# Kernel tuning notes

Measured on AMD Instinct MI355X. Metric: run time of the kernel, lower is better.

## Reference

```python
import jax, jax.numpy as jnp
import numpy as np

SEQ = 4096
D_EMB = 2048
D_HEAD = 128
SCALE = 0.02


def setup_inputs() -> dict:
    key = jax.random.key(0)
    kx, kq, kk, kv, ko = jax.random.split(key, 5)
    x = jax.random.normal(kx, (SEQ, D_EMB), dtype=jnp.float32)
    W_Q = jax.random.normal(kq, (D_EMB, D_EMB), dtype=jnp.float32) * SCALE
    W_K = jax.random.normal(kk, (D_EMB, D_EMB), dtype=jnp.float32) * SCALE
    W_V = jax.random.normal(kv, (D_EMB, D_EMB), dtype=jnp.float32) * SCALE
    W_O = jax.random.normal(ko, (D_EMB, D_EMB), dtype=jnp.float32) * SCALE
    b_Q = jnp.zeros((D_EMB,), dtype=jnp.float32)
    b_K = jnp.zeros((D_EMB,), dtype=jnp.float32)
    b_V = jnp.zeros((D_EMB,), dtype=jnp.float32)
    b_O = jnp.zeros((D_EMB,), dtype=jnp.float32)
    return {"x": x, "W_Q": W_Q, "W_K": W_K, "W_V": W_V, "W_O": W_O,
            "b_Q": b_Q, "b_K": b_K, "b_V": b_V, "b_O": b_O, "d_head": D_HEAD}


def reference(x, W_Q, W_K, W_V, W_O, b_Q, b_K, b_V, b_O, d_head):
    # x: [S, D]
    q = x @ W_Q + b_Q  # [S, D]
    k = x @ W_K + b_K
    v = x @ W_V + b_V
    scores = (q @ k.T) / jnp.sqrt(jnp.float32(d_head))  # [S, S]
    seq = scores.shape[0]
    causal = jnp.tril(jnp.ones((seq, seq), dtype=bool))
    scores = jnp.where(causal, scores, -jnp.inf)
    weights = jax.nn.softmax(scores, axis=-1)  # [S, S]
    attn_out = weights @ v  # [S, D]
    return attn_out @ W_O + b_O
```

## Files before the change

### kernel.cpp

```cpp
#include <hip/hip_runtime.h>
#include <hip/hip_fp16.h>

typedef _Float16 f16;
typedef _Float16 f16x8 __attribute__((ext_vector_type(8)));
typedef _Float16 f16x4 __attribute__((ext_vector_type(4)));
typedef float    f32x4 __attribute__((ext_vector_type(4)));

#define SEQ      4096
#define DEMB     2048
#define SCALE_QK 0.08838834764831845f

#define GAS __attribute__((address_space(1)))
#define LAS __attribute__((address_space(3)))

__device__ __forceinline__ void load_lds16(const f16* g, f16* l) {
    __builtin_amdgcn_global_load_lds((const GAS void*)g, (LAS void*)l, 16, 0, 0);
}

__device__ __forceinline__ f16x8 ldsr(const f16* base, int byteoff) {
    byteoff ^= (byteoff >> 3) & 0x70;
    return *(const f16x8*)((const char*)base + byteoff);
}

__device__ __forceinline__ void stage_half(const f16* __restrict__ src, int ldk,
                                           f16* ldsdst, int tid) {
#pragma unroll
    for (int s = 0; s < 2; ++s) {
        const int o   = s * 8192 + tid * 16;
        const int osw = o ^ ((o >> 3) & 0x70);
        load_lds16(src + (size_t)(osw >> 7) * ldk + ((osw & 127) >> 1),
                   ldsdst + (s * 8192 + (tid >> 6) * 1024) / 2);
    }
}

template <int MODE>
__device__ __forceinline__ void gemm_core(
        const f16* __restrict__ A, int lda, const f16* __restrict__ BT, int ldb,
        void* __restrict__ outp, int ldo, const float* __restrict__ bias,
        int bm, int bn, int NTc, int kt0, float scale, f16* lds) {
    const int m0 = bm * 256, n0 = bn * 256;
    const int NI = NTc >> 1;

    const int tid  = threadIdx.x;
    const int lane = tid & 63;
    const int wr   = (tid >> 6) >> 2;
    const int wc   = (tid >> 6) & 3;
    const int fr   = lane & 15;
    const int kb   = (lane >> 4) * 16;

    const f16* Abase = A + (size_t)m0 * lda + kt0 * 64;
    const f16* Bbase = BT + (size_t)n0 * ldb + kt0 * 64;

#define STG(buf, isB, half, t) \
    stage_half((isB) ? (Bbase + (size_t)((half) * 128) * ldb + (t) * 64) \
                     : (Abase + (size_t)((half) * 128) * lda + (t) * 64), \
               (isB) ? ldb : lda, \
               lds + (buf) * 32768 + (isB) * 16384 + (half) * 8192, tid)

    f32x4 acc[8][4] = {};
    f16x8 af[8], bf0[4], bf1[4];

#define READ_A(Mh, buf) { \
    const f16* bb = lds + (buf) * 32768; \
    _Pragma("unroll") for (int m = 0; m < 4; ++m) \
    _Pragma("unroll") for (int ks = 0; ks < 2; ++ks) \
        af[m * 2 + ks] = ldsr(bb, ((Mh) * 128 + wr * 64 + m * 16 + fr) * 128 + ks * 64 + kb); }

#define READ_B(Nh, buf, dst) { \
    const f16* bb = lds + (buf) * 32768 + 16384; \
    _Pragma("unroll") for (int n = 0; n < 2; ++n) \
    _Pragma("unroll") for (int ks = 0; ks < 2; ++ks) \
        dst[n * 2 + ks] = ldsr(bb, ((Nh) * 128 + wc * 32 + n * 16 + fr) * 128 + ks * 64 + kb); }

#define MFMA_PH(Mh, Nh, bfx) { \
    __builtin_amdgcn_s_setprio(1); \
    _Pragma("unroll") for (int m = 0; m < 4; ++m) \
    _Pragma("unroll") for (int n = 0; n < 2; ++n) \
    _Pragma("unroll") for (int ks = 0; ks < 2; ++ks) \
        acc[(Mh) * 4 + m][(Nh) * 2 + n] = __builtin_amdgcn_mfma_f32_16x16x32_f16( \
            af[m * 2 + ks], bfx[n * 2 + ks], acc[(Mh) * 4 + m][(Nh) * 2 + n], 0, 0, 0); \
    __builtin_amdgcn_s_setprio(0); }

#define BAR   asm volatile("s_barrier" ::: "memory")
#define VM6   asm volatile("s_waitcnt vmcnt(6)" ::: "memory")
#define VM0   asm volatile("s_waitcnt vmcnt(0)" ::: "memory")

    STG(0, 0, 0, 0); STG(0, 1, 0, 0); STG(0, 1, 1, 0); STG(0, 0, 1, 0);
    STG(1, 0, 0, 1); STG(1, 1, 0, 1); STG(1, 1, 1, 1);
    VM6; BAR;

    for (int i = 0; i < NI; ++i) {
        const int t0 = 2 * i;
        const bool more = (i + 1 < NI);
        READ_A(0, 0); READ_B(0, 0, bf0);
        STG(1, 0, 1, t0 + 1);
        BAR; MFMA_PH(0, 0, bf0); BAR;
        READ_B(1, 0, bf1);
        if (more) STG(0, 0, 0, t0 + 2);
        BAR; MFMA_PH(0, 1, bf1); BAR;
        READ_A(1, 0);
        if (more) STG(0, 1, 0, t0 + 2);
        BAR; MFMA_PH(1, 0, bf0); BAR;
        if (more) { STG(0, 1, 1, t0 + 2); VM6; } else { VM0; }
        BAR; MFMA_PH(1, 1, bf1); BAR;
        READ_A(0, 1); READ_B(0, 1, bf0);
        if (more) STG(0, 0, 1, t0 + 2);
        BAR; MFMA_PH(0, 0, bf0); BAR;
        READ_B(1, 1, bf1);
        if (more) STG(1, 0, 0, t0 + 3);
        BAR; MFMA_PH(0, 1, bf1); BAR;
        READ_A(1, 1);
        if (more) STG(1, 1, 0, t0 + 3);
        BAR; MFMA_PH(1, 0, bf0); BAR;
        if (more) STG(1, 1, 1, t0 + 3);
        VM6;
        BAR; MFMA_PH(1, 1, bf1); BAR;
    }

    const int rq = (lane >> 4) * 4;
#pragma unroll
    for (int mi = 0; mi < 8; ++mi) {
        const int row = m0 + (mi >> 2) * 128 + wr * 64 + (mi & 3) * 16 + rq;
#pragma unroll
        for (int ni = 0; ni < 4; ++ni) {
            const int col = n0 + (ni >> 1) * 128 + wc * 32 + (ni & 1) * 16 + fr;
            if (MODE == 0) {
                f16* o = (f16*)outp;
                const float bv = bias[col];
#pragma unroll
                for (int r = 0; r < 4; ++r)
                    o[(size_t)(row + r) * ldo + col] = (f16)(acc[mi][ni][r] + bv);
            } else if (MODE == 1) {
                f16* o = (f16*)outp;
                f16x4 v;
#pragma unroll
                for (int r = 0; r < 4; ++r) v[r] = (f16)acc[mi][ni][r];
                *(f16x4*)&o[(size_t)col * ldo + row] = v;
            } else if (MODE == 2) {
                float* o = (float*)outp;
                const float bv = bias ? bias[col] : 0.f;
#pragma unroll
                for (int r = 0; r < 4; ++r)
                    atomicAdd(&o[(size_t)(row + r) * ldo + col], acc[mi][ni][r] + bv);
            } else {
                f16* o = (f16*)outp;
#pragma unroll
                for (int r = 0; r < 4; ++r)
                    o[(size_t)(row + r) * ldo + col] = (f16)(acc[mi][ni][r] * scale);
            }
        }
    }
#undef STG
#undef READ_A
#undef READ_B
#undef MFMA_PH
#undef BAR
#undef VM6
#undef VM0
}

__global__ __launch_bounds__(256) void cvt_f16(const float* __restrict__ in,
                                               f16* __restrict__ out, int n) {
    int i = (blockIdx.x * 256 + threadIdx.x) * 4;
    if (i >= n) return;
    float4 v = *(const float4*)&in[i];
    f16x4 o; o[0] = (f16)v.x; o[1] = (f16)v.y; o[2] = (f16)v.z; o[3] = (f16)v.w;
    *(f16x4*)&out[i] = o;
}

__global__ __launch_bounds__(256) void transpose_cvt4(
        const float* __restrict__ WQ, const float* __restrict__ WK,
        const float* __restrict__ WV, const float* __restrict__ WO,
        f16* __restrict__ wqkvt, f16* __restrict__ wot) {
    __shared__ f16 tile[64][72];
    const int z = blockIdx.z;
    const float* in = z == 0 ? WQ : z == 1 ? WK : z == 2 ? WV : WO;
    f16* out = z < 3 ? wqkvt + (size_t)z * DEMB * DEMB : wot;
    const int c0 = blockIdx.x * 64, r0 = blockIdx.y * 64;
    const int tx = threadIdx.x & 63, ty = threadIdx.x >> 6;
    for (int rr = ty; rr < 64; rr += 4)
        tile[tx][rr] = (f16)in[(size_t)(r0 + rr) * DEMB + c0 + tx];
    __syncthreads();
    for (int cc = ty; cc < 64; cc += 4)
        out[(size_t)(c0 + cc) * DEMB + r0 + tx] = tile[cc][tx];
}

__global__ __launch_bounds__(512, 2)
void k_qkv(const f16* __restrict__ x16, const f16* __restrict__ wqkvt,
           f16* __restrict__ qkv16, const float* __restrict__ bqkv) {
    __shared__ f16 lds[65536];
    gemm_core<0>(x16, DEMB, wqkvt, DEMB, qkv16, 3 * DEMB, bqkv,
                 blockIdx.y, blockIdx.x, 32, 0, 1.f, lds);
}

__global__ __launch_bounds__(512, 2)
void k_scores(const f16* __restrict__ qkv16, f16* __restrict__ sb) {
    __shared__ f16 lds[65536];
    const int bid = blockIdx.x;
    int bm = (int)((sqrtf(8.f * bid + 1.f) - 1.f) * 0.5f);
    while ((bm + 1) * (bm + 2) / 2 <= bid) ++bm;
    while (bm * (bm + 1) / 2 > bid) --bm;
    const int bn = bid - bm * (bm + 1) / 2;
    gemm_core<3>(qkv16, 3 * DEMB, qkv16 + DEMB, 3 * DEMB, sb, SEQ, nullptr,
                 bm, bn, 32, 0, SCALE_QK, lds);
}

__global__ __launch_bounds__(512, 2)
void k_vw_softmax(const f16* __restrict__ qkv16, const f16* __restrict__ wot,
                  f16* __restrict__ vwT, f16* __restrict__ sb) {
    __shared__ f16 lds[65536];
    const int bid = blockIdx.x;
    if (bid < 128) {
        gemm_core<1>(qkv16 + 2 * DEMB, 3 * DEMB, wot, DEMB, vwT, SEQ, nullptr,
                     bid >> 3, bid & 7, 32, 0, 1.f, lds);
        return;
    }
    f16* srow = lds + (size_t)(threadIdx.x >> 8) * SEQ;
    float* red = (float*)(lds + 2 * SEQ);
    const int half = threadIdx.x >> 8;
    const int tt   = threadIdx.x & 255;
    const int i    = 2 * (bid - 128) + half;
    const int L    = i + 1;
    const int Lp   = ((i >> 8) + 1) << 8;
    f16* row = sb + (size_t)i * SEQ;

    float mx = -3.0e38f;
    for (int j0 = tt * 8; j0 < Lp; j0 += 2048) {
        f16x8 v = *(const f16x8*)&row[j0];
        *(f16x8*)&srow[j0] = v;
#pragma unroll
        for (int u = 0; u < 8; ++u)
            if (j0 + u < L) mx = fmaxf(mx, (float)v[u]);
    }
#pragma unroll
    for (int o = 32; o > 0; o >>= 1) mx = fmaxf(mx, __shfl_xor(mx, o));
    if ((tt & 63) == 0) red[half * 8 + (tt >> 6)] = mx;
    __syncthreads();
    mx = fmaxf(fmaxf(red[half * 8 + 0], red[half * 8 + 1]),
               fmaxf(red[half * 8 + 2], red[half * 8 + 3]));

    float sm = 0.f;
    for (int j0 = tt * 8; j0 < Lp; j0 += 2048) {
        f16x8 v = *(const f16x8*)&srow[j0];
#pragma unroll
        for (int u = 0; u < 8; ++u)
            if (j0 + u < L) sm += __expf((float)v[u] - mx);
    }
#pragma unroll
    for (int o = 32; o > 0; o >>= 1) sm += __shfl_xor(sm, o);
    if ((tt & 63) == 0) red[half * 8 + 4 + (tt >> 6)] = sm;
    __syncthreads();
    const float inv = 1.f / (red[half * 8 + 4] + red[half * 8 + 5] +
                             red[half * 8 + 6] + red[half * 8 + 7]);

    for (int j0 = tt * 8; j0 < Lp; j0 += 2048) {
        f16x8 v = *(const f16x8*)&srow[j0];
        f16x8 wv;
#pragma unroll
        for (int u = 0; u < 8; ++u)
            wv[u] = (j0 + u < L) ? (f16)(__expf((float)v[u] - mx) * inv) : (f16)0.f;
        *(f16x8*)&row[j0] = wv;
    }
}

__global__ __launch_bounds__(512, 2)
void k_pvw(const f16* __restrict__ sb, const f16* __restrict__ vwT,
           float* __restrict__ out, const float* __restrict__ bO) {
    __shared__ f16 lds[65536];
    const int bm = blockIdx.y, bn = blockIdx.x, z = blockIdx.z;
    const int NT = (bm + 1) * 4;
    const int half = NT >> 1;
    gemm_core<2>(sb, SEQ, vwT, SEQ, out, DEMB, z == 0 ? bO : nullptr,
                 bm, bn, half, z * half, 1.f, lds);
}

extern "C" void kernel_launch(void* const* d_in, const int* in_sizes, int n_in,
                              void* d_out, int out_size, void* d_ws, size_t ws_size,
                              hipStream_t stream) {
    const float* x  = (const float*)d_in[0];
    const float* WQ = (const float*)d_in[1];
    const float* WK = (const float*)d_in[2];
    const float* WV = (const float*)d_in[3];
    const float* WO = (const float*)d_in[4];
    const float* bQ = (const float*)d_in[5];
    const float* bK = (const float*)d_in[6];
    const float* bV = (const float*)d_in[7];
    const float* bO = (const float*)d_in[8];
    float* out = (float*)d_out;

    char* w = (char*)d_ws;
    f16* qkv16 = (f16*)w; w += (size_t)SEQ * 3 * DEMB * 2;
    f16* vwT   = (f16*)w; w += (size_t)DEMB * SEQ * 2;
    f16* wot   = (f16*)w; w += (size_t)DEMB * DEMB * 2;
    float* bqkv = (float*)w; w += 3 * DEMB * 4 + 8192;
    char* R = w;
    f16* x16   = (f16*)R;
    f16* wqkvt = (f16*)(R + (size_t)SEQ * DEMB * 2);
    f16* sb    = (f16*)R;

    cvt_f16<<<(SEQ * DEMB) / 1024, 256, 0, stream>>>(x, x16, SEQ * DEMB);
    transpose_cvt4<<<dim3(DEMB / 64, DEMB / 64, 4), 256, 0, stream>>>(
        WQ, WK, WV, WO, wqkvt, wot);
    hipMemcpyAsync(bqkv, bQ, DEMB * 4, hipMemcpyDeviceToDevice, stream);
    hipMemcpyAsync(bqkv + DEMB, bK, DEMB * 4, hipMemcpyDeviceToDevice, stream);
    hipMemcpyAsync(bqkv + 2 * DEMB, bV, DEMB * 4, hipMemcpyDeviceToDevice, stream);

    k_qkv<<<dim3(3 * DEMB / 256, SEQ / 256), 512, 0, stream>>>(
        x16, wqkvt, qkv16, bqkv);

    k_scores<<<136, 512, 0, stream>>>(qkv16, sb);

    k_vw_softmax<<<128 + SEQ / 2, 512, 0, stream>>>(qkv16, wot, vwT, sb);

    hipMemsetAsync(out, 0, (size_t)SEQ * DEMB * 4, stream);
    k_pvw<<<dim3(DEMB / 256, SEQ / 256, 2), 512, 0, stream>>>(sb, vwT, out, bO);
}
```

Measured before the change: 347.2 us.

## Fold W_V into W_O product and balance causal PV split across blocks

```diff
diff --git a/kernel.cpp b/kernel.cpp
--- a/kernel.cpp
+++ b/kernel.cpp
@@ -37,9 +37,8 @@
 __device__ __forceinline__ void gemm_core(
         const f16* __restrict__ A, int lda, const f16* __restrict__ BT, int ldb,
         void* __restrict__ outp, int ldo, const float* __restrict__ bias,
-        int bm, int bn, int NTc, int kt0, float scale, f16* lds) {
+        int bm, int bn, int NI, int kt0, float scale, f16* lds) {
     const int m0 = bm * 256, n0 = bn * 256;
-    const int NI = NTc >> 1;
 
     const int tid  = threadIdx.x;
     const int lane = tid & 63;
@@ -168,14 +167,14 @@
     *(f16x4*)&out[i] = o;
 }
 
-__global__ __launch_bounds__(256) void transpose_cvt4(
+__global__ __launch_bounds__(256) void transpose_cvt3(
         const float* __restrict__ WQ, const float* __restrict__ WK,
-        const float* __restrict__ WV, const float* __restrict__ WO,
-        f16* __restrict__ wqkvt, f16* __restrict__ wot) {
+        const float* __restrict__ WO,
+        f16* __restrict__ wqkt, f16* __restrict__ wot) {
     __shared__ f16 tile[64][72];
     const int z = blockIdx.z;
-    const float* in = z == 0 ? WQ : z == 1 ? WK : z == 2 ? WV : WO;
-    f16* out = z < 3 ? wqkvt + (size_t)z * DEMB * DEMB : wot;
+    const float* in = z == 0 ? WQ : z == 1 ? WK : WO;
+    f16* out = z == 0 ? wqkt : z == 1 ? wqkt + (size_t)DEMB * DEMB : wot;
     const int c0 = blockIdx.x * 64, r0 = blockIdx.y * 64;
     const int tx = threadIdx.x & 63, ty = threadIdx.x >> 6;
     for (int rr = ty; rr < 64; rr += 4)
@@ -186,33 +185,56 @@
 }
 
 __global__ __launch_bounds__(512, 2)
-void k_qkv(const f16* __restrict__ x16, const f16* __restrict__ wqkvt,
-           f16* __restrict__ qkv16, const float* __restrict__ bqkv) {
+void k_qk(const f16* __restrict__ x16, const f16* __restrict__ wqkt,
+          f16* __restrict__ qk16, const float* __restrict__ bqk) {
     __shared__ f16 lds[65536];
-    gemm_core<0>(x16, DEMB, wqkvt, DEMB, qkv16, 3 * DEMB, bqkv,
-                 blockIdx.y, blockIdx.x, 32, 0, 1.f, lds);
+    gemm_core<0>(x16, DEMB, wqkt, DEMB, qk16, 2 * DEMB, bqk,
+                 blockIdx.y, blockIdx.x, 16, 0, 1.f, lds);
 }
 
 __global__ __launch_bounds__(512, 2)
-void k_scores(const f16* __restrict__ qkv16, f16* __restrict__ sb) {
+void k_scores_wvo(const f16* __restrict__ qk16, f16* __restrict__ sb,
+                  const f16* __restrict__ wv16, const f16* __restrict__ wot,
+                  f16* __restrict__ wvoT) {
     __shared__ f16 lds[65536];
     const int bid = blockIdx.x;
-    int bm = (int)((sqrtf(8.f * bid + 1.f) - 1.f) * 0.5f);
-    while ((bm + 1) * (bm + 2) / 2 <= bid) ++bm;
-    while (bm * (bm + 1) / 2 > bid) --bm;
-    const int bn = bid - bm * (bm + 1) / 2;
-    gemm_core<3>(qkv16, 3 * DEMB, qkv16 + DEMB, 3 * DEMB, sb, SEQ, nullptr,
-                 bm, bn, 32, 0, SCALE_QK, lds);
+    if (bid < 136) {
+        int bm = (int)((sqrtf(8.f * bid + 1.f) - 1.f) * 0.5f);
+        while ((bm + 1) * (bm + 2) / 2 <= bid) ++bm;
+        while (bm * (bm + 1) / 2 > bid) --bm;
+        const int bn = bid - bm * (bm + 1) / 2;
+        gemm_core<3>(qk16, 2 * DEMB, qk16 + DEMB, 2 * DEMB, sb, SEQ, nullptr,
+                     bm, bn, 16, 0, SCALE_QK, lds);
+    } else {
+        const int w = bid - 136;
+        gemm_core<1>(wv16, DEMB, wot, DEMB, wvoT, DEMB, nullptr,
+                     w >> 3, w & 7, 16, 0, 1.f, lds);
+    }
 }
 
 __global__ __launch_bounds__(512, 2)
-void k_vw_softmax(const f16* __restrict__ qkv16, const f16* __restrict__ wot,
-                  f16* __restrict__ vwT, f16* __restrict__ sb) {
+void k_vw_sm_bias(const f16* __restrict__ x16, const f16* __restrict__ wvoT,
+                  f16* __restrict__ vwT, f16* __restrict__ sb,
+                  const float* __restrict__ WO, const float* __restrict__ bV,
+                  const float* __restrict__ bO, float* __restrict__ bc) {
     __shared__ f16 lds[65536];
     const int bid = blockIdx.x;
     if (bid < 128) {
-        gemm_core<1>(qkv16 + 2 * DEMB, 3 * DEMB, wot, DEMB, vwT, SEQ, nullptr,
-                     bid >> 3, bid & 7, 32, 0, 1.f, lds);
+        gemm_core<1>(x16, DEMB, wvoT, DEMB, vwT, SEQ, nullptr,
+                     bid >> 3, bid & 7, 16, 0, 1.f, lds);
+        return;
+    }
+    if (bid >= 2176) {
+        float* part = (float*)lds;
+        const int j0 = (bid - 2176) * 256;
+        const int jj = threadIdx.x & 255;
+        const int hf = threadIdx.x >> 8;
+        float acc = 0.f;
+        for (int i = hf * 1024; i < (hf + 1) * 1024; ++i)
+            acc += bV[i] * WO[(size_t)i * DEMB + j0 + jj];
+        part[hf * 256 + jj] = acc;
+        __syncthreads();
+        if (hf == 0) bc[j0 + jj] = part[jj] + part[256 + jj] + bO[j0 + jj];
         return;
     }
     f16* srow = lds + (size_t)(threadIdx.x >> 8) * SEQ;
@@ -265,13 +287,18 @@
 
 __global__ __launch_bounds__(512, 2)
 void k_pvw(const f16* __restrict__ sb, const f16* __restrict__ vwT,
-           float* __restrict__ out, const float* __restrict__ bO) {
+           float* __restrict__ out, const float* __restrict__ bc) {
     __shared__ f16 lds[65536];
-    const int bm = blockIdx.y, bn = blockIdx.x, z = blockIdx.z;
-    const int NT = (bm + 1) * 4;
-    const int half = NT >> 1;
-    gemm_core<2>(sb, SEQ, vwT, SEQ, out, DEMB, z == 0 ? bO : nullptr,
-                 bm, bn, half, z * half, 1.f, lds);
+    static const short BMt[30] = {0,1,2,3,4,5,6,6,7,7,8,8,9,9,10,10,11,11,
+                                  12,12,12,13,13,13,14,14,14,15,15,15};
+    static const short KT0t[30] = {0,0,0,0,0,0,0,14,0,16,0,18,0,20,0,22,0,24,
+                                   0,18,36,0,20,38,0,20,40,0,22,44};
+    static const short NIt[30] = {2,4,6,8,10,12,7,7,8,8,9,9,10,10,11,11,12,12,
+                                  9,9,8,10,9,9,10,10,10,11,11,10};
+    const int e = blockIdx.x, bn = blockIdx.y;
+    const int bm = BMt[e], kt0 = KT0t[e], ni = NIt[e];
+    gemm_core<2>(sb, SEQ, vwT, SEQ, out, DEMB, kt0 == 0 ? bc : nullptr,
+                 bm, bn, ni, kt0, 1.f, lds);
 }
 
 extern "C" void kernel_launch(void* const* d_in, const int* in_sizes, int n_in,
@@ -289,29 +316,31 @@
     float* out = (float*)d_out;
 
     char* w = (char*)d_ws;
-    f16* qkv16 = (f16*)w; w += (size_t)SEQ * 3 * DEMB * 2;
-    f16* vwT   = (f16*)w; w += (size_t)DEMB * SEQ * 2;
-    f16* wot   = (f16*)w; w += (size_t)DEMB * DEMB * 2;
-    float* bqkv = (float*)w; w += 3 * DEMB * 4 + 8192;
-    char* R = w;
-    f16* x16   = (f16*)R;
-    f16* wqkvt = (f16*)(R + (size_t)SEQ * DEMB * 2);
-    f16* sb    = (f16*)R;
+    f16* qk16 = (f16*)w; w += (size_t)SEQ * 2 * DEMB * 2;
+    f16* sb   = (f16*)w; w += (size_t)SEQ * SEQ * 2;
+    f16* x16  = (f16*)w; w += (size_t)SEQ * DEMB * 2;
+    f16* wqkt = (f16*)w; w += (size_t)2 * DEMB * DEMB * 2;
+    f16* wv16 = (f16*)w; w += (size_t)DEMB * DEMB * 2;
+    f16* wot  = (f16*)w; w += (size_t)DEMB * DEMB * 2;
+    f16* wvoT = (f16*)w; w += (size_t)DEMB * DEMB * 2;
+    float* bqk = (float*)w; w += 2 * DEMB * 4;
+    float* bc  = (float*)w; w += DEMB * 4 + 4096;
+    f16* vwT = wqkt;
 
     cvt_f16<<<(SEQ * DEMB) / 1024, 256, 0, stream>>>(x, x16, SEQ * DEMB);
-    transpose_cvt4<<<dim3(DEMB / 64, DEMB / 64, 4), 256, 0, stream>>>(
-        WQ, WK, WV, WO, wqkvt, wot);
-    hipMemcpyAsync(bqkv, bQ, DEMB * 4, hipMemcpyDeviceToDevice, stream);
-    hipMemcpyAsync(bqkv + DEMB, bK, DEMB * 4, hipMemcpyDeviceToDevice, stream);
-    hipMemcpyAsync(bqkv + 2 * DEMB, bV, DEMB * 4, hipMemcpyDeviceToDevice, stream);
-
-    k_qkv<<<dim3(3 * DEMB / 256, SEQ / 256), 512, 0, stream>>>(
-        x16, wqkvt, qkv16, bqkv);
-
-    k_scores<<<136, 512, 0, stream>>>(qkv16, sb);
-
-    k_vw_softmax<<<128 + SEQ / 2, 512, 0, stream>>>(qkv16, wot, vwT, sb);
+    cvt_f16<<<(DEMB * DEMB) / 1024, 256, 0, stream>>>(WV, wv16, DEMB * DEMB);
+    transpose_cvt3<<<dim3(DEMB / 64, DEMB / 64, 3), 256, 0, stream>>>(
+        WQ, WK, WO, wqkt, wot);
+    hipMemcpyAsync(bqk, bQ, DEMB * 4, hipMemcpyDeviceToDevice, stream);
+    hipMemcpyAsync(bqk + DEMB, bK, DEMB * 4, hipMemcpyDeviceToDevice, stream);
+
+    k_qk<<<dim3(2 * DEMB / 256, SEQ / 256), 512, 0, stream>>>(
+        x16, wqkt, qk16, bqk);
+
+    k_scores_wvo<<<200, 512, 0, stream>>>(qk16, sb, wv16, wot, wvoT);
+
+    k_vw_sm_bias<<<2184, 512, 0, stream>>>(x16, wvoT, vwT, sb, WO, bV, bO, bc);
 
     hipMemsetAsync(out, 0, (size_t)SEQ * DEMB * 4, stream);
-    k_pvw<<<dim3(DEMB / 256, SEQ / 256, 2), 512, 0, stream>>>(sb, vwT, out, bO);
-}
+    k_pvw<<<dim3(30, 8), 512, 0, stream>>>(sb, vwT, out, bc);
+}
```

After: 546.7 us. +57.5%, slower.
